# Kernel tuning notes

Measured on AMD Instinct MI355X. Metric: run time of the kernel, lower is better.

The kernel has to match this reference:

```python
import jax, jax.numpy as jnp
import numpy as np

C = 1536
MA = 1536
NEG_SLOPE = 0.2


def setup_inputs() -> dict:
    key = jax.random.key(0)
    ks = jax.random.split(key, 11)
    s = 1.0 / np.sqrt(C)

    def u(k, shape):
        return jax.random.uniform(k, shape, jnp.float32, -s, s)

    return {
        "x": jax.random.normal(ks[0], (1, C), jnp.float32),
        "lw0": u(ks[1], (C, C)), "lb0": u(ks[2], (C,)),
        "lw1": u(ks[3], (C, C)), "lb1": u(ks[4], (C,)),
        "lw2": u(ks[5], (1, C)), "lb2": u(ks[6], (1,)),
        "W_ih": u(ks[7], (3, C, C)), "b_ih": u(ks[8], (3, C)),
        "W_hh": u(ks[9], (3, C, C)), "b_hh": u(ks[10], (3, C)),
        "max_atoms": MA,
    }


def reference(x, lw0, lb0, lw1, lb1, lw2, lb2, W_ih, b_ih, W_hh, b_hh, max_atoms):
    c_dim = x.shape[-1]
    x = x.reshape(1, c_dim)

    act = lambda v: jax.nn.leaky_relu(v, NEG_SLOPE)
    # LinearOutputStack(channels, 3, out_channels=1): 2 hidden layers + output head
    h = act(x @ lw0.T + lb0)
    h = act(h @ lw1.T + lb1)
    l = h @ lw2.T + lb2                       # [1, 1]
    length = jnp.clip(jnp.abs(l), 0.0, 0.9999)
    c = jnp.floor(length[0, 0] * max_atoms).astype(jnp.int32) + 1  # #valid steps

    hid0 = jnp.zeros((3, c_dim), x.dtype).at[0].set(x[0])  # hid[0] = x
    inp0 = jnp.zeros((c_dim,), x.dtype)

    def step(carry, _):
        inp, hid = carry
        cur = inp
        new_hid = []
        for layer in range(3):  # stacked relu-RNN, one timestep
            nh = jax.nn.relu(cur @ W_ih[layer].T + b_ih[layer]
                             + hid[layer] @ W_hh[layer].T + b_hh[layer])
            new_hid.append(nh)
            cur = nh
        return (cur, jnp.stack(new_hid)), cur

    _, seq = jax.lax.scan(step, (inp0, hid0), None, length=max_atoms)  # [MA, C]
    # Original returns only the first c rows; we pad with zeros for static shape.
    mask = (jnp.arange(max_atoms) < c)[:, None]
    seq = jnp.where(mask, seq, jnp.zeros((), seq.dtype))
    return seq, length
```

## Files before the change

### kernel.cpp

```cpp
#include <hip/hip_runtime.h>
#include <math.h>

#define C     1536
#define MA    1536
#define NWG   256
#define TPB   384
#define NEG   0.2f

typedef unsigned long long u64;

#define WS_H0    0
#define WS_H1    (C)
#define WS_HB    (2*C)
#define WS_CNUM  (6*C)
#define WS_ARR   (6*C + 64)

#define WSCALE   (32760.0f * 39.191835884530846f)
#define WINV     (1.0f / WSCALE)

#define WL_WORDS (36 * 768)

__global__ void ve_init(unsigned* w) {
    for (int k = threadIdx.x; k < NWG * 16; k += blockDim.x)
        __hip_atomic_store(&w[WS_ARR + k], 0u, __ATOMIC_RELAXED, __HIP_MEMORY_SCOPE_AGENT);
}

__device__ __forceinline__ float wave_reduce(float v) {
#pragma unroll
    for (int off = 32; off > 0; off >>= 1) v += __shfl_xor(v, off, 64);
    return v;
}
__device__ __forceinline__ unsigned aloadu(const unsigned* p) {
    return __hip_atomic_load(p, __ATOMIC_RELAXED, __HIP_MEMORY_SCOPE_AGENT);
}
__device__ __forceinline__ u64 aload64(const u64* p) {
    return __hip_atomic_load(p, __ATOMIC_RELAXED, __HIP_MEMORY_SCOPE_AGENT);
}

__device__ __forceinline__ float dot_row64(const float* __restrict__ W,
                                           const float* __restrict__ v, int lane) {
    const float4* W4 = (const float4*)W;
    const float4* v4 = (const float4*)v;
    float acc = 0.f;
#pragma unroll
    for (int j = 0; j < 6; ++j) {
        float4 a = W4[lane + 64 * j];
        float4 b = v4[lane + 64 * j];
        acc = fmaf(a.x, b.x, acc); acc = fmaf(a.y, b.y, acc);
        acc = fmaf(a.z, b.z, acc); acc = fmaf(a.w, b.w, acc);
    }
    return acc;
}

__device__ __forceinline__ float dot_i16(const int* __restrict__ wrow,
                                         const float* __restrict__ h, int lane) {
    float acc = 0.f;
#pragma unroll
    for (int mm = 0; mm < 12; ++mm) {
        int w = wrow[mm * 64 + lane];
        float2 hv = *(const float2*)(h + 2 * (mm * 64 + lane));
        acc = fmaf((float)(short)w, hv.x, acc);
        acc = fmaf((float)(w >> 16), hv.y, acc);
    }
    return acc;
}

__device__ __forceinline__ void stage_h(const float* __restrict__ hsrc,
                                        float* __restrict__ hdst, int wave, int lane) {
    const u64* p = (const u64*)hsrc;
    const int i0 = wave * 128 + lane;
    const int i1 = i0 + 64;
    u64 a = aload64(p + i0);
    u64 b = aload64(p + i1);
    union { u64 u; float2 f; } ua, ub;
    ua.u = a; ub.u = b;
    ((float2*)hdst)[i0] = ua.f;
    ((float2*)hdst)[i1] = ub.f;
}

__device__ __forceinline__ void bar_all(unsigned* arr, unsigned ep) {
    __syncthreads();
    if (threadIdx.x == 0) {
        __hip_atomic_store(arr + blockIdx.x * 16, ep, __ATOMIC_RELAXED, __HIP_MEMORY_SCOPE_AGENT);
        __builtin_amdgcn_fence(__ATOMIC_ACQUIRE, "agent");
    }
    if (threadIdx.x < 64) {
        const int i = threadIdx.x;
        unsigned m;
        do {
            unsigned f0 = aloadu(arr + (i      ) * 16);
            unsigned f1 = aloadu(arr + (i +  64) * 16);
            unsigned f2 = aloadu(arr + (i + 128) * 16);
            unsigned f3 = aloadu(arr + (i + 192) * 16);
            m = min(min(f0, f1), min(f2, f3));
            if (m < ep) __builtin_amdgcn_s_sleep(1);
        } while (m < ep);
    }
    __syncthreads();
}

extern __shared__ int wldsi[];

__global__ void __launch_bounds__(TPB, 1)
ve_main(const float* __restrict__ x,
        const float* __restrict__ lw0, const float* __restrict__ lb0,
        const float* __restrict__ lw1, const float* __restrict__ lb1,
        const float* __restrict__ lw2, const float* __restrict__ lb2,
        const float* __restrict__ Wih, const float* __restrict__ bih,
        const float* __restrict__ Whh, const float* __restrict__ bhh,
        float* __restrict__ out, float* __restrict__ wsf) {
    unsigned* wsu = (unsigned*)wsf;
    int*      wsi = (int*)wsf;
    unsigned* arr = wsu + WS_ARR;
    float*    hb  = wsf + WS_HB;
    float*    Lring = (float*)(wldsi + WL_WORDS);
    const int tid  = threadIdx.x;
    const int b    = blockIdx.x;
    const int wave = tid >> 6;
    const int lane = tid & 63;
    const int row  = b * 6 + wave;

#pragma unroll
    for (int lm = 0; lm < 6; ++lm) {
        const int l = lm >> 1, m = lm & 1;
        const float* src = (m == 0 ? Wih : Whh) + ((size_t)l * C + row) * C;
        int* dst = wldsi + (lm * 6 + wave) * 768;
#pragma unroll
        for (int mm = 0; mm < 12; ++mm) {
            const int i = mm * 64 + lane;
            float2 wv = *(const float2*)(src + 2 * i);
            int q0 = (int)rintf(wv.x * WSCALE);
            int q1 = (int)rintf(wv.y * WSCALE);
            dst[i] = (q0 & 0xFFFF) | (q1 << 16);
        }
    }
    float bsum[3];
#pragma unroll
    for (int l = 0; l < 3; ++l) bsum[l] = bih[l * C + row] + bhh[l * C + row];

    {
        const int gtid = b * TPB + tid;
        if (gtid < 3 * C) {
            int slot = 1 + gtid / C;
            int idx  = gtid % C;
            float v  = (slot == 1) ? x[idx] : 0.f;
            __hip_atomic_store(&hb[slot * C + idx], v, __ATOMIC_RELAXED, __HIP_MEMORY_SCOPE_AGENT);
        }
    }

    {
        const int i0 = wave * 128 + lane;
        const int i1 = i0 + 64;
        const float2* xs = (const float2*)x;
        ((float2*)(Lring + 1 * 1536))[i0] = xs[i0];
        ((float2*)(Lring + 1 * 1536))[i1] = xs[i1];
        float2 z2 = make_float2(0.f, 0.f);
        ((float2*)(Lring + 2 * 1536))[i0] = z2;
        ((float2*)(Lring + 2 * 1536))[i1] = z2;
    }

    {
        float acc = wave_reduce(dot_row64(lw0 + (size_t)row * C, x, lane));
        if (lane == 0) {
            float v = acc + lb0[row];
            v = (v > 0.f) ? v : NEG * v;
            __hip_atomic_store(&wsf[WS_H0 + row], v, __ATOMIC_RELAXED, __HIP_MEMORY_SCOPE_AGENT);
        }
    }
    bar_all(arr, 1);
    {
        float acc = wave_reduce(dot_row64(lw1 + (size_t)row * C, wsf + WS_H0, lane));
        if (lane == 0) {
            float v = acc + lb1[row];
            v = (v > 0.f) ? v : NEG * v;
            __hip_atomic_store(&wsf[WS_H1 + row], v, __ATOMIC_RELAXED, __HIP_MEMORY_SCOPE_AGENT);
        }
    }
    bar_all(arr, 2);
    if (row == 0) {
        float acc = wave_reduce(dot_row64(lw2, wsf + WS_H1, lane));
        if (lane == 0) {
            float l = acc + lb2[0];
            float length = fminf(fabsf(l), 0.9999f);
            __hip_atomic_store(&out[(size_t)MA * C], length, __ATOMIC_RELAXED,
                               __HIP_MEMORY_SCOPE_AGENT);
            __hip_atomic_store(&wsi[WS_CNUM], (int)floorf(length * (float)MA) + 1,
                               __ATOMIC_RELAXED, __HIP_MEMORY_SCOPE_AGENT);
        }
    }
    bar_all(arr, 3);
    const int csteps = wsi[WS_CNUM];

    int k = 0;
    for (int t = 0; t < csteps; ++t) {
#pragma unroll
        for (int l = 0; l < 3; ++l, ++k) {
            const int* wh = wldsi + ((l * 2 + 1) * 6 + wave) * 768;
            float hh_acc = dot_i16(wh, Lring + ((l + 1) % 3) * 1536, lane);
            if (tid < 64) {
                const unsigned* p = arr + tid * 16;
                const unsigned target = 3 + (unsigned)k;
                unsigned m;
                do {
                    unsigned f0 = aloadu(p);
                    unsigned f1 = aloadu(p +  64 * 16);
                    unsigned f2 = aloadu(p + 128 * 16);
                    unsigned f3 = aloadu(p + 192 * 16);
                    m = min(min(f0, f1), min(f2, f3));
                    if (m < target) __builtin_amdgcn_s_sleep(1);
                } while (m < target);
            }
            __syncthreads();
            stage_h(hb + ((k - 1) & 3) * C, Lring + l * 1536, wave, lane);
            __syncthreads();
            float vout;
            {
                const int* wi = wldsi + ((l * 2 + 0) * 6 + wave) * 768;
                float acc = hh_acc + dot_i16(wi, Lring + l * 1536, lane);
                acc = wave_reduce(acc);
                vout = fmaxf(fmaf(acc, WINV, bsum[l]), 0.f);
                if (lane == 0)
                    __hip_atomic_store(&hb[(k & 3) * C + row], vout, __ATOMIC_RELAXED,
                                       __HIP_MEMORY_SCOPE_AGENT);
            }
            __syncthreads();
            if (tid == 0)
                __hip_atomic_store(arr + b * 16, 4 + (unsigned)k, __ATOMIC_RELAXED,
                                   __HIP_MEMORY_SCOPE_AGENT);
            if (l == 2 && lane == 0) out[(size_t)t * C + row] = vout;
        }
    }
}

extern "C" void kernel_launch(void* const* d_in, const int* in_sizes, int n_in,
                              void* d_out, int out_size, void* d_ws, size_t ws_size,
                              hipStream_t stream) {
    const float* x   = (const float*)d_in[0];
    const float* lw0 = (const float*)d_in[1];
    const float* lb0 = (const float*)d_in[2];
    const float* lw1 = (const float*)d_in[3];
    const float* lb1 = (const float*)d_in[4];
    const float* lw2 = (const float*)d_in[5];
    const float* lb2 = (const float*)d_in[6];
    const float* Wih = (const float*)d_in[7];
    const float* bih = (const float*)d_in[8];
    const float* Whh = (const float*)d_in[9];
    const float* bhh = (const float*)d_in[10];
    float* out = (float*)d_out;
    float* wsf = (float*)d_ws;

    const int lds_bytes = WL_WORDS * 4 + 3 * 1536 * 4;
    hipFuncSetAttribute((const void*)ve_main,
                        hipFuncAttributeMaxDynamicSharedMemorySize, lds_bytes);

    hipMemsetAsync(d_out, 0, (size_t)out_size * sizeof(float), stream);
    hipLaunchKernelGGL(ve_init, dim3(1), dim3(256), 0, stream, (unsigned*)d_ws);

    void* args[] = {
        (void*)&x, (void*)&lw0, (void*)&lb0, (void*)&lw1, (void*)&lb1,
        (void*)&lw2, (void*)&lb2, (void*)&Wih, (void*)&bih, (void*)&Whh,
        (void*)&bhh, (void*)&out, (void*)&wsf
    };
    hipLaunchCooperativeKernel((const void*)ve_main, dim3(NWG), dim3(TPB),
                               args, lds_bytes, stream);
}
```

Measured before the change: 430.7 us.

## Replace per-block arrival flag with per-wave flags to drop trailing block barrier

Each wave now publishes its own readiness flag (six per block, packed in one cache line) right after storing its hidden-state output, with a vmcnt wait so the data store lands before the flag. The __syncthreads before a single per-block flag store is removed. Pollers read each line with three 64-bit loads and take the min of the six flags. This shortens the critical path of the grid-wide sync at every RNN step. In exchange the poll loop does more loads, and ordering now depends on the waitcnt, not on a release fence.

```diff
diff --git a/kernel.cpp b/kernel.cpp
--- a/kernel.cpp
+++ b/kernel.cpp
@@ -14,6 +14,7 @@
 #define WS_HB    (2*C)
 #define WS_CNUM  (6*C)
 #define WS_ARR   (6*C + 64)
+#define WS_RF    (WS_ARR + NWG*16)
 
 #define WSCALE   (32760.0f * 39.191835884530846f)
 #define WINV     (1.0f / WSCALE)
@@ -21,7 +22,7 @@
 #define WL_WORDS (36 * 768)
 
 __global__ void ve_init(unsigned* w) {
-    for (int k = threadIdx.x; k < NWG * 16; k += blockDim.x)
+    for (int k = threadIdx.x; k < 2 * NWG * 16; k += blockDim.x)
         __hip_atomic_store(&w[WS_ARR + k], 0u, __ATOMIC_RELAXED, __HIP_MEMORY_SCOPE_AGENT);
 }
 
@@ -99,6 +100,16 @@
     __syncthreads();
 }
 
+__device__ __forceinline__ unsigned line_min6(const unsigned* line) {
+    u64 a = aload64((const u64*)line);
+    u64 b = aload64((const u64*)line + 1);
+    u64 c = aload64((const u64*)line + 2);
+    unsigned m = min((unsigned)a, (unsigned)(a >> 32));
+    m = min(m, min((unsigned)b, (unsigned)(b >> 32)));
+    m = min(m, min((unsigned)c, (unsigned)(c >> 32)));
+    return m;
+}
+
 extern __shared__ int wldsi[];
 
 __global__ void __launch_bounds__(TPB, 1)
@@ -112,6 +123,7 @@
     unsigned* wsu = (unsigned*)wsf;
     int*      wsi = (int*)wsf;
     unsigned* arr = wsu + WS_ARR;
+    unsigned* rf  = wsu + WS_RF;
     float*    hb  = wsf + WS_HB;
     float*    Lring = (float*)(wldsi + WL_WORDS);
     const int tid  = threadIdx.x;
@@ -190,6 +202,7 @@
     }
     bar_all(arr, 3);
     const int csteps = wsi[WS_CNUM];
+    __syncthreads();
 
     int k = 0;
     for (int t = 0; t < csteps; ++t) {
@@ -197,37 +210,35 @@
         for (int l = 0; l < 3; ++l, ++k) {
             const int* wh = wldsi + ((l * 2 + 1) * 6 + wave) * 768;
             float hh_acc = dot_i16(wh, Lring + ((l + 1) % 3) * 1536, lane);
-            if (tid < 64) {
-                const unsigned* p = arr + tid * 16;
-                const unsigned target = 3 + (unsigned)k;
+            if (k > 0 && tid < 64) {
+                const unsigned target = (unsigned)k;
                 unsigned m;
                 do {
-                    unsigned f0 = aloadu(p);
-                    unsigned f1 = aloadu(p +  64 * 16);
-                    unsigned f2 = aloadu(p + 128 * 16);
-                    unsigned f3 = aloadu(p + 192 * 16);
-                    m = min(min(f0, f1), min(f2, f3));
+                    unsigned m0 = line_min6(rf + (tid      ) * 16);
+                    unsigned m1 = line_min6(rf + (tid +  64) * 16);
+                    unsigned m2 = line_min6(rf + (tid + 128) * 16);
+                    unsigned m3 = line_min6(rf + (tid + 192) * 16);
+                    m = min(min(m0, m1), min(m2, m3));
                     if (m < target) __builtin_amdgcn_s_sleep(1);
                 } while (m < target);
             }
             __syncthreads();
             stage_h(hb + ((k - 1) & 3) * C, Lring + l * 1536, wave, lane);
             __syncthreads();
-            float vout;
             {
                 const int* wi = wldsi + ((l * 2 + 0) * 6 + wave) * 768;
                 float acc = hh_acc + dot_i16(wi, Lring + l * 1536, lane);
                 acc = wave_reduce(acc);
-                vout = fmaxf(fmaf(acc, WINV, bsum[l]), 0.f);
+                float vout = fmaxf(fmaf(acc, WINV, bsum[l]), 0.f);
                 if (lane == 0)
                     __hip_atomic_store(&hb[(k & 3) * C + row], vout, __ATOMIC_RELAXED,
                                        __HIP_MEMORY_SCOPE_AGENT);
+                asm volatile("s_waitcnt vmcnt(0)" ::: "memory");
+                if (lane == 0)
+                    __hip_atomic_store(&rf[b * 16 + wave], (unsigned)(k + 1), __ATOMIC_RELAXED,
+                                       __HIP_MEMORY_SCOPE_AGENT);
+                if (l == 2 && lane == 0) out[(size_t)t * C + row] = vout;
             }
-            __syncthreads();
-            if (tid == 0)
-                __hip_atomic_store(arr + b * 16, 4 + (unsigned)k, __ATOMIC_RELAXED,
-                                   __HIP_MEMORY_SCOPE_AGENT);
-            if (l == 2 && lane == 0) out[(size_t)t * C + row] = vout;
         }
     }
 }
```

Result: slower. 1.124 ms (+160.9%).
